# Performance work log

Measured on AMD Instinct MI355X. Metric: run time of the kernel, lower is better.

Reference implementation:

```python
import jax, jax.numpy as jnp
import numpy as np

D = 1024
H = 16
DH = D // H
F = 4096
B, S = 4, 2048
EPS = 1e-5


def _ln(x, g, b):
    m = jnp.mean(x, axis=-1, keepdims=True)
    v = jnp.var(x, axis=-1, keepdims=True)
    return (x - m) * jax.lax.rsqrt(v + EPS) * g + b


def setup_inputs() -> dict:
    key = jax.random.key(0)
    ks = jax.random.split(key, 16)
    s = 0.02
    return {
        "x": jax.random.normal(ks[0], (B, S, D), jnp.float32),
        "key_padding_mask": jnp.zeros((B, S), jnp.bool_),
        "Wq": jax.random.normal(ks[1], (D, D), jnp.float32) * s,
        "bq": jnp.zeros((D,), jnp.float32),
        "Wk": jax.random.normal(ks[2], (D, D), jnp.float32) * s,
        "bk": jnp.zeros((D,), jnp.float32),
        "Wv": jax.random.normal(ks[3], (D, D), jnp.float32) * s,
        "bv": jnp.zeros((D,), jnp.float32),
        "Wo": jax.random.normal(ks[4], (D, D), jnp.float32) * s,
        "bo": jnp.zeros((D,), jnp.float32),
        "W1": jax.random.normal(ks[5], (F, D), jnp.float32) * s,
        "b1": jnp.zeros((F,), jnp.float32),
        "W2": jax.random.normal(ks[6], (D, F), jnp.float32) * s,
        "b2": jnp.zeros((D,), jnp.float32),
        "ln1_g": jnp.ones((D,), jnp.float32),
        "ln1_b": jnp.zeros((D,), jnp.float32),
        "ln2_g": jnp.ones((D,), jnp.float32),
        "ln2_b": jnp.zeros((D,), jnp.float32),
    }


def _attn(x, kpm, Wq, bq, Wk, bk, Wv, bv, Wo, bo):
    b, s, d = x.shape
    scaling = DH ** (-0.5)
    q = (x @ Wq.T + bq) * scaling
    k = x @ Wk.T + bk
    v = x @ Wv.T + bv
    q = q.reshape(b, s, H, DH)
    k = k.reshape(b, s, H, DH)
    v = v.reshape(b, s, H, DH)
    # [b,h,q,k]
    scores = jnp.einsum("bqhd,bkhd->bhqk", q, k)
    scores = jnp.where(kpm[:, None, None, :], -jnp.inf, scores)
    p = jax.nn.softmax(scores.astype(jnp.float32), axis=-1).astype(q.dtype)
    out = jnp.einsum("bhqk,bkhd->bqhd", p, v).reshape(b, s, d)
    return out @ Wo.T + bo


def reference(x, key_padding_mask, Wq, bq, Wk, bk, Wv, bv, Wo, bo,
              W1, b1, W2, b2, ln1_g, ln1_b, ln2_g, ln2_b):
    # post-LN (normalize_before=False), dropout in eval mode (identity)
    x = _ln(x + _attn(x, key_padding_mask, Wq, bq, Wk, bk, Wv, bv, Wo, bo), ln1_g, ln1_b)
    h = jax.nn.gelu(x @ W1.T + b1, approximate=False)
    x = _ln(x + (h @ W2.T + b2), ln2_g, ln2_b)
    return x
```

## Files before the change

kernel.cpp:

```cpp
#include <hip/hip_runtime.h>
#include <hip/hip_bf16.h>
#include <math.h>

typedef short bf16x8 __attribute__((ext_vector_type(8)));
typedef float f32x4 __attribute__((ext_vector_type(4)));

__device__ __forceinline__ unsigned short f2bfu(float f) {
    __hip_bfloat16 h = __float2bfloat16(f);
    return __builtin_bit_cast(unsigned short, h);
}

__device__ __forceinline__ float fexp2(float x) {
    float r;
    asm("v_exp_f32 %0, %1" : "=v"(r) : "v"(x));
    return r;
}

__device__ __forceinline__ unsigned cvtpk_bf16(float lo, float hi) {
    unsigned r;
    asm("v_cvt_pk_bf16_f32 %0, %1, %2" : "=v"(r) : "v"(lo), "v"(hi));
    return r;
}

__device__ __forceinline__ float gelu_fast(float x) {
    const float x2 = x * x;
    const float z = x * (0.7978845608f + 0.0356774081f * x2);
    const float e = fexp2(z * 2.88539008f);
    const float r = __builtin_amdgcn_rcpf(e + 1.0f);
    return x * (1.0f - r);
}

__device__ __forceinline__ void gload_lds16(const void* gsrc, void* ldst) {
    __builtin_amdgcn_global_load_lds((const __attribute__((address_space(1))) void*)gsrc,
                                     (__attribute__((address_space(3))) void*)ldst,
                                     16, 0, 0);
}

__global__ __launch_bounds__(256)
void cvt_bf16_kernel(const float4* __restrict__ in, ushort4* __restrict__ out, int n4) {
    int i = blockIdx.x * 256 + threadIdx.x;
    if (i >= n4) return;
    float4 v = in[i];
    ushort4 o;
    o.x = f2bfu(v.x); o.y = f2bfu(v.y); o.z = f2bfu(v.z); o.w = f2bfu(v.w);
    out[i] = o;
}

enum { EPI_QKV = 0, EPI_RESF32 = 2, EPI_GELU = 3, EPI_RESBF16 = 5 };

template<int EPI>
__global__ __launch_bounds__(256, 2)
void gemm_bt(const __hip_bfloat16* __restrict__ A,
             const __hip_bfloat16* __restrict__ W,
             const float* __restrict__ bias,
             const void* __restrict__ resv,
             float scale,
             void* __restrict__ outp, void* __restrict__ outp2, void* __restrict__ outp3,
             int M, int N, int K)
{
    __shared__ __hip_bfloat16 As[2][128 * 32];
    __shared__ __hip_bfloat16 Ws[2][128 * 32];
    const int tid = threadIdx.x;
    const int lane = tid & 63;
    const int wid = tid >> 6;
    const int wr = wid >> 1, wc = wid & 1;
    const int g = lane >> 4, lr = lane & 15;
    const int row0 = blockIdx.x * 128;
    const int col0 = blockIdx.y * 128;

    f32x4 acc[4][4];
    const f32x4 zero = {0.f, 0.f, 0.f, 0.f};
#pragma unroll
    for (int m = 0; m < 4; ++m)
#pragma unroll
        for (int n = 0; n < 4; ++n) acc[m][n] = zero;

    const int c0 = tid, c1 = tid + 256;
    const int ar0 = c0 >> 2, ar1 = c1 >> 2;
    const int ac0 = ((c0 & 3) ^ ((ar0 >> 1) & 3)) * 8;
    const int ac1 = ((c1 & 3) ^ ((ar1 >> 1) & 3)) * 8;
    const __hip_bfloat16* Arow0 = A + (size_t)(row0 + ar0) * K + ac0;
    const __hip_bfloat16* Arow1 = A + (size_t)(row0 + ar1) * K + ac1;
    const __hip_bfloat16* Wrow0 = W + (size_t)(col0 + ar0) * K + ac0;
    const __hip_bfloat16* Wrow1 = W + (size_t)(col0 + ar1) * K + ac1;

    auto stage = [&](int bi, int k0) {
        gload_lds16(Arow0 + k0, (char*)As[bi] + c0 * 16);
        gload_lds16(Arow1 + k0, (char*)As[bi] + c1 * 16);
        gload_lds16(Wrow0 + k0, (char*)Ws[bi] + c0 * 16);
        gload_lds16(Wrow1 + k0, (char*)Ws[bi] + c1 * 16);
    };

    stage(0, 0);
    __syncthreads();
    int buf = 0;
    const int NT = K >> 5;
    const int swl = (lr >> 1) & 3;

    for (int t = 0; t < NT; ++t) {
        if (t + 1 < NT) stage(buf ^ 1, (t + 1) * 32);
        bf16x8 af[4], wf[4];
#pragma unroll
        for (int m = 0; m < 4; ++m)
            af[m] = *(const bf16x8*)(As[buf] + (wr * 64 + m * 16 + lr) * 32 + (g ^ swl) * 8);
#pragma unroll
        for (int n = 0; n < 4; ++n)
            wf[n] = *(const bf16x8*)(Ws[buf] + (wc * 64 + n * 16 + lr) * 32 + (g ^ swl) * 8);
#pragma unroll
        for (int m = 0; m < 4; ++m)
#pragma unroll
            for (int n = 0; n < 4; ++n)
                acc[m][n] = __builtin_amdgcn_mfma_f32_16x16x32_bf16(af[m], wf[n], acc[m][n], 0, 0, 0);
        __syncthreads();
        buf ^= 1;
    }

#pragma unroll
    for (int n = 0; n < 4; ++n) {
        const int cc = col0 + wc * 64 + n * 16 + lr;
        const float bv = bias[cc];
#pragma unroll
        for (int m = 0; m < 4; ++m) {
            const int rbase = row0 + wr * 64 + m * 16 + g * 4;
            if (EPI == EPI_QKV) {
                const int seg = col0 >> 10;
                if (seg == 2) {
                    ushort4 u;
                    u.x = f2bfu(acc[m][n][0] + bv);
                    u.y = f2bfu(acc[m][n][1] + bv);
                    u.z = f2bfu(acc[m][n][2] + bv);
                    u.w = f2bfu(acc[m][n][3] + bv);
                    const int cc2 = cc - 2048;
                    const int h_ = cc2 >> 6, dh = cc2 & 63;
                    const int bb = rbase >> 11;
                    const int s = rbase & 2047;
                    *(ushort4*)((__hip_bfloat16*)outp3 +
                                (((size_t)bb * 16 + h_) * 64 + dh) * 2048 + s) = u;
                } else {
                    const float sc = (seg == 0) ? scale : 1.0f;
                    __hip_bfloat16* dst = (seg == 0) ? (__hip_bfloat16*)outp
                                                     : (__hip_bfloat16*)outp2;
                    const int ccl = cc & 1023;
#pragma unroll
                    for (int r = 0; r < 4; ++r)
                        dst[(size_t)(rbase + r) * 1024 + ccl] =
                            __float2bfloat16((acc[m][n][r] + bv) * sc);
                }
            } else {
#pragma unroll
                for (int r = 0; r < 4; ++r) {
                    const size_t idx = (size_t)(rbase + r) * N + cc;
                    float v = acc[m][n][r] + bv;
                    if (EPI == EPI_RESF32) {
                        ((float*)outp)[idx] = v + ((const float*)resv)[idx];
                    } else if (EPI == EPI_RESBF16) {
                        ((float*)outp)[idx] = v +
                            __bfloat162float(((const __hip_bfloat16*)resv)[idx]);
                    } else if (EPI == EPI_GELU) {
                        ((__hip_bfloat16*)outp)[idx] = __float2bfloat16(gelu_fast(v));
                    }
                }
            }
        }
    }
}

__global__ __launch_bounds__(256, 2)
void attn_flash2(const __hip_bfloat16* __restrict__ Q,
                 const __hip_bfloat16* __restrict__ K,
                 const __hip_bfloat16* __restrict__ VT,
                 const unsigned char* __restrict__ kpm,
                 __hip_bfloat16* __restrict__ O)
{
    __shared__ __hip_bfloat16 Ks[2][64 * 64];
    __shared__ __hip_bfloat16 VTs[2][64 * 64];
    __shared__ __hip_bfloat16 Plds[4][64 * 64];

    const int tid = threadIdx.x;
    const int lane = tid & 63;
    const int w = tid >> 6;
    const int g = lane >> 4, lr = lane & 15;

    const int orig = blockIdx.y * 8 + blockIdx.x;
    const int nl = (orig & 7) * 64 + (orig >> 3);
    const int qb = nl & 7;
    const int bh = nl >> 3;

    const int b = bh >> 4, h = bh & 15;
    const int q0 = qb * 256 + w * 64;
    const size_t tokbase = (size_t)b * 2048;
    const __hip_bfloat16* VTbh = VT + (size_t)bh * 64 * 2048;

    bf16x8 qf[4][2];
#pragma unroll
    for (int qn = 0; qn < 4; ++qn)
#pragma unroll
        for (int f = 0; f < 2; ++f)
            qf[qn][f] = *(const bf16x8*)(Q + (tokbase + q0 + qn * 16 + lr) * 1024 +
                                         h * 64 + f * 32 + g * 8);

    f32x4 o[4][4];
    const f32x4 zero = {0.f, 0.f, 0.f, 0.f};
#pragma unroll
    for (int qa = 0; qa < 4; ++qa)
#pragma unroll
        for (int nd = 0; nd < 4; ++nd) o[qa][nd] = zero;
    float m_run[4], l_part[4];
#pragma unroll
    for (int qn = 0; qn < 4; ++qn) { m_run[qn] = -1e30f; l_part[qn] = 0.f; }

    __hip_bfloat16* Pw = Plds[w];
    const int rowl = lane >> 3;
    const int blkp = lane & 7;

    auto stage = [&](int bufi, int kv0) {
#pragma unroll
        for (int iss = 0; iss < 2; ++iss) {
            const int row = w * 16 + iss * 8 + rowl;
            const int sblk = blkp ^ (row & 7);
            gload_lds16(K + (tokbase + kv0 + row) * 1024 + h * 64 + sblk * 8,
                        (char*)&Ks[bufi][(w * 16 + iss * 8) * 64] + (lane & 63) * 16);
            gload_lds16(VTbh + (size_t)row * 2048 + kv0 + sblk * 8,
                        (char*)&VTs[bufi][(w * 16 + iss * 8) * 64] + (lane & 63) * 16);
        }
    };

    stage(0, 0);
    __syncthreads();
    int buf = 0;

    for (int t = 0; t < 32; ++t) {
        const int kv0 = t * 64;
        if (t < 31) stage(buf ^ 1, kv0 + 64);

        f32x4 st[4][4];
        __builtin_amdgcn_s_setprio(1);
#pragma unroll
        for (int km = 0; km < 4; ++km) {
            bf16x8 kf[2];
#pragma unroll
            for (int f = 0; f < 2; ++f)
                kf[f] = *(const bf16x8*)(&Ks[buf][(km * 16 + lr) * 64 +
                                                  (((f * 4 + g) ^ (lr & 7)) * 8)]);
#pragma unroll
            for (int qn = 0; qn < 4; ++qn) {
                st[km][qn] = __builtin_amdgcn_mfma_f32_16x16x32_bf16(kf[0], qf[qn][0], zero, 0, 0, 0);
                st[km][qn] = __builtin_amdgcn_mfma_f32_16x16x32_bf16(kf[1], qf[qn][1], st[km][qn], 0, 0, 0);
            }
        }
        __builtin_amdgcn_s_setprio(0);

        if (__any((int)(kpm[tokbase + kv0 + lane] != 0))) {
            const float NEG = -1e30f;
#pragma unroll
            for (int km = 0; km < 4; ++km) {
                const unsigned mu = *(const unsigned*)(kpm + tokbase + kv0 + km * 16 + g * 4);
#pragma unroll
                for (int r = 0; r < 4; ++r) {
                    if ((mu >> (8 * r)) & 0xFFu) {
#pragma unroll
                        for (int qn = 0; qn < 4; ++qn) st[km][qn][r] = NEG;
                    }
                }
            }
        }

        float pm[4];
#pragma unroll
        for (int qn = 0; qn < 4; ++qn) {
            float a0 = fmaxf(fmaxf(st[0][qn][0], st[0][qn][1]), fmaxf(st[0][qn][2], st[0][qn][3]));
            float a1 = fmaxf(fmaxf(st[1][qn][0], st[1][qn][1]), fmaxf(st[1][qn][2], st[1][qn][3]));
            float a2 = fmaxf(fmaxf(st[2][qn][0], st[2][qn][1]), fmaxf(st[2][qn][2], st[2][qn][3]));
            float a3 = fmaxf(fmaxf(st[3][qn][0], st[3][qn][1]), fmaxf(st[3][qn][2], st[3][qn][3]));
            pm[qn] = fmaxf(fmaxf(a0, a1), fmaxf(a2, a3));
        }
        const int trig = (pm[0] > m_run[0] + 8.f) | (pm[1] > m_run[1] + 8.f) |
                         (pm[2] > m_run[2] + 8.f) | (pm[3] > m_run[3] + 8.f);
        if (__any(trig)) {
            float alpha_q[4];
#pragma unroll
            for (int qn = 0; qn < 4; ++qn) {
                float rm = pm[qn];
                rm = fmaxf(rm, __shfl_xor(rm, 16));
                rm = fmaxf(rm, __shfl_xor(rm, 32));
                const float mnew = fmaxf(m_run[qn], rm);
                const float al = fexp2(m_run[qn] - mnew);
                l_part[qn] *= al;
                m_run[qn] = mnew;
                alpha_q[qn] = al;
            }
#pragma unroll
            for (int qa = 0; qa < 4; ++qa)
#pragma unroll
                for (int r = 0; r < 4; ++r) {
                    const float av = __shfl(alpha_q[qa], g * 4 + r, 16);
#pragma unroll
                    for (int nd = 0; nd < 4; ++nd) o[qa][nd][r] *= av;
                }
        }

#pragma unroll
        for (int qn = 0; qn < 4; ++qn) {
            const float mm = m_run[qn];
#pragma unroll
            for (int km = 0; km < 4; ++km) {
                const float p0 = fexp2(st[km][qn][0] - mm);
                const float p1 = fexp2(st[km][qn][1] - mm);
                const float p2 = fexp2(st[km][qn][2] - mm);
                const float p3 = fexp2(st[km][qn][3] - mm);
                l_part[qn] += (p0 + p1) + (p2 + p3);
                uint2 pk;
                pk.x = cvtpk_bf16(p0, p1);
                pk.y = cvtpk_bf16(p2, p3);
                const int cs = (km * 2 + (g >> 1)) ^ (lr & 7);
                *(uint2*)(Pw + (qn * 16 + lr) * 64 + cs * 8 + (g & 1) * 4) = pk;
            }
        }

        __builtin_amdgcn_s_setprio(1);
#pragma unroll
        for (int f = 0; f < 2; ++f) {
            bf16x8 pa[4];
#pragma unroll
            for (int qa = 0; qa < 4; ++qa)
                pa[qa] = *(const bf16x8*)(Pw + (qa * 16 + lr) * 64 +
                                          (((f * 4 + g) ^ (lr & 7)) * 8));
#pragma unroll
            for (int nd = 0; nd < 4; ++nd) {
                bf16x8 vb = *(const bf16x8*)(&VTs[buf][(nd * 16 + lr) * 64 +
                                                       (((f * 4 + g) ^ (lr & 7)) * 8)]);
#pragma unroll
                for (int qa = 0; qa < 4; ++qa)
                    o[qa][nd] = __builtin_amdgcn_mfma_f32_16x16x32_bf16(pa[qa], vb, o[qa][nd], 0, 0, 0);
            }
        }
        __builtin_amdgcn_s_setprio(0);

        __syncthreads();
        buf ^= 1;
    }

    float linv[4];
#pragma unroll
    for (int qn = 0; qn < 4; ++qn) {
        float lt = l_part[qn];
        lt += __shfl_xor(lt, 16);
        lt += __shfl_xor(lt, 32);
        linv[qn] = 1.0f / lt;
    }
#pragma unroll
    for (int qa = 0; qa < 4; ++qa)
#pragma unroll
        for (int r = 0; r < 4; ++r) {
            const float lv = __shfl(linv[qa], g * 4 + r, 16);
            const size_t row = tokbase + q0 + qa * 16 + g * 4 + r;
#pragma unroll
            for (int nd = 0; nd < 4; ++nd)
                O[row * 1024 + h * 64 + nd * 16 + lr] = __float2bfloat16(o[qa][nd][r] * lv);
        }
}

__global__ __launch_bounds__(256)
void ln_kernel(const float* __restrict__ in, const float* __restrict__ gamma,
               const float* __restrict__ beta, float* __restrict__ outf,
               __hip_bfloat16* __restrict__ outb)
{
    const int row = blockIdx.x;
    const int tid = threadIdx.x;
    float4 v = ((const float4*)(in + (size_t)row * 1024))[tid];
    float s = v.x + v.y + v.z + v.w;
    float s2 = v.x * v.x + v.y * v.y + v.z * v.z + v.w * v.w;
#pragma unroll
    for (int off = 1; off < 64; off <<= 1) {
        s += __shfl_xor(s, off);
        s2 += __shfl_xor(s2, off);
    }
    __shared__ float red[8];
    const int wv = tid >> 6;
    if ((tid & 63) == 0) { red[wv] = s; red[4 + wv] = s2; }
    __syncthreads();
    s = red[0] + red[1] + red[2] + red[3];
    s2 = red[4] + red[5] + red[6] + red[7];
    const float mean = s * (1.f / 1024.f);
    const float var = s2 * (1.f / 1024.f) - mean * mean;
    const float rstd = rsqrtf(var + 1e-5f);
    float4 gm = ((const float4*)gamma)[tid];
    float4 bt = ((const float4*)beta)[tid];
    float4 y;
    y.x = (v.x - mean) * rstd * gm.x + bt.x;
    y.y = (v.y - mean) * rstd * gm.y + bt.y;
    y.z = (v.z - mean) * rstd * gm.z + bt.z;
    y.w = (v.w - mean) * rstd * gm.w + bt.w;
    if (outf) ((float4*)(outf + (size_t)row * 1024))[tid] = y;
    if (outb) {
        ushort4 ub;
        ub.x = f2bfu(y.x); ub.y = f2bfu(y.y); ub.z = f2bfu(y.z); ub.w = f2bfu(y.w);
        ((ushort4*)outb)[row * 256 + tid] = ub;
    }
}

extern "C" void kernel_launch(void* const* d_in, const int* in_sizes, int n_in,
                              void* d_out, int out_size, void* d_ws, size_t ws_size,
                              hipStream_t stream)
{
    const float* x    = (const float*)d_in[0];
    const unsigned char* kpm = (const unsigned char*)d_in[1];
    const float* Wq = (const float*)d_in[2];
    const float* bq = (const float*)d_in[3];
    const float* Wk = (const float*)d_in[4];
    const float* bk = (const float*)d_in[5];
    const float* Wv = (const float*)d_in[6];
    const float* bv = (const float*)d_in[7];
    const float* Wo = (const float*)d_in[8];
    const float* bo = (const float*)d_in[9];
    const float* W1 = (const float*)d_in[10];
    const float* b1 = (const float*)d_in[11];
    const float* W2 = (const float*)d_in[12];
    const float* b2 = (const float*)d_in[13];
    const float* ln1g = (const float*)d_in[14];
    const float* ln1b = (const float*)d_in[15];
    const float* ln2g = (const float*)d_in[16];
    const float* ln2b = (const float*)d_in[17];
    float* out = (float*)d_out;

    char* ws = (char*)d_ws;
    const size_t SZ_ND2 = (size_t)8192 * 1024 * 2;
    size_t off = 0;
    __hip_bfloat16* xb  = (__hip_bfloat16*)(ws + off); off += SZ_ND2;
    __hip_bfloat16* wqb = (__hip_bfloat16*)(ws + off); off += (size_t)1024 * 1024 * 2;
    __hip_bfloat16* wkb = (__hip_bfloat16*)(ws + off); off += (size_t)1024 * 1024 * 2;
    __hip_bfloat16* wvb = (__hip_bfloat16*)(ws + off); off += (size_t)1024 * 1024 * 2;
    __hip_bfloat16* wob = (__hip_bfloat16*)(ws + off); off += (size_t)1024 * 1024 * 2;
    __hip_bfloat16* w1b = (__hip_bfloat16*)(ws + off); off += (size_t)4096 * 1024 * 2;
    __hip_bfloat16* w2b = (__hip_bfloat16*)(ws + off); off += (size_t)4096 * 1024 * 2;
    const size_t qkv0 = off;
    __hip_bfloat16* qbp = (__hip_bfloat16*)(ws + off); off += SZ_ND2;
    __hip_bfloat16* kbp = (__hip_bfloat16*)(ws + off); off += SZ_ND2;
    __hip_bfloat16* vtg = (__hip_bfloat16*)(ws + off); off += SZ_ND2;
    __hip_bfloat16* abp = (__hip_bfloat16*)(ws + off); off += SZ_ND2;
    __hip_bfloat16* hbp = (__hip_bfloat16*)(ws + qkv0);
    float* y1 = (float*)(ws + off); off += (size_t)8192 * 1024 * 4;
    __hip_bfloat16* x1b = (__hip_bfloat16*)(ws + off); off += SZ_ND2;
    float* y2 = y1;

    float* bqkv = (float*)(ws + off); off += 3072 * 4;

    auto cvt = [&](const float* src, void* dst, int n) {
        cvt_bf16_kernel<<<n / 1024, 256, 0, stream>>>((const float4*)src, (ushort4*)dst, n / 4);
    };
    cvt(x,  xb,  8192 * 1024);
    cvt(Wq, wqb, 1024 * 1024);
    cvt(Wk, wkb, 1024 * 1024);
    cvt(Wv, wvb, 1024 * 1024);
    cvt(Wo, wob, 1024 * 1024);
    cvt(W1, w1b, 4096 * 1024);
    cvt(W2, w2b, 4096 * 1024);
    hipMemcpyAsync(bqkv,        bq, 4096, hipMemcpyDeviceToDevice, stream);
    hipMemcpyAsync(bqkv + 1024, bk, 4096, hipMemcpyDeviceToDevice, stream);
    hipMemcpyAsync(bqkv + 2048, bv, 4096, hipMemcpyDeviceToDevice, stream);

    dim3 blk(256);

    const float qscale = 0.125f * 1.44269504088896f;
    gemm_bt<EPI_QKV><<<dim3(64, 24), blk, 0, stream>>>(
        xb, wqb, bqkv, nullptr, qscale, qbp, kbp, vtg, 8192, 3072, 1024);

    attn_flash2<<<dim3(8, 64), blk, 0, stream>>>(qbp, kbp, vtg, kpm, abp);

    gemm_bt<EPI_RESF32><<<dim3(64, 8), blk, 0, stream>>>(
        abp, wob, bo, x, 1.0f, y1, nullptr, nullptr, 8192, 1024, 1024);
    ln_kernel<<<8192, 256, 0, stream>>>(y1, ln1g, ln1b, nullptr, x1b);

    gemm_bt<EPI_GELU><<<dim3(64, 32), blk, 0, stream>>>(
        x1b, w1b, b1, nullptr, 1.0f, hbp, nullptr, nullptr, 8192, 4096, 1024);
    gemm_bt<EPI_RESBF16><<<dim3(64, 8), blk, 0, stream>>>(
        hbp, w2b, b2, x1b, 1.0f, y2, nullptr, nullptr, 8192, 1024, 4096);
    ln_kernel<<<8192, 256, 0, stream>>>(y2, ln2g, ln2b, out, nullptr);
}
```

Before: 446.1 us.

## Add 256x256 tiled GEMM kernel with interleaved LDS staging for QKV and FFN

Introduces a 512-thread GEMM kernel computing 256x256 output tiles with a K-step of 64. It overlaps direct global-to-LDS loads of the next A/B tiles with MFMA quadrants, using explicit barriers, waitcnt and priority hints. The QKV, FFN1 and FFN2 GEMMs switch to this kernel to raise arithmetic intensity and hide load latency. In exchange it needs much more LDS per block and launches far fewer blocks, which may underfill the GPU for the narrow FFN2 output.

After: 485.5 us. 1.09x slower.

```diff
diff --git a/kernel.cpp b/kernel.cpp
--- a/kernel.cpp
+++ b/kernel.cpp
@@ -35,6 +35,8 @@
                                      (__attribute__((address_space(3))) void*)ldst,
                                      16, 0, 0);
 }
+
+#define MFMA __builtin_amdgcn_mfma_f32_16x16x32_bf16
 
 __global__ __launch_bounds__(256)
 void cvt_bf16_kernel(const float4* __restrict__ in, ushort4* __restrict__ out, int n4) {
@@ -47,6 +49,199 @@
 }
 
 enum { EPI_QKV = 0, EPI_RESF32 = 2, EPI_GELU = 3, EPI_RESBF16 = 5 };
+
+template<int EPI>
+__global__ __launch_bounds__(512, 2)
+void gemm256(const __hip_bfloat16* __restrict__ A,
+             const __hip_bfloat16* __restrict__ W,
+             const float* __restrict__ bias,
+             const void* __restrict__ resv,
+             float scale,
+             void* __restrict__ outp, void* __restrict__ outp2, void* __restrict__ outp3,
+             int M, int N, int K)
+{
+    __shared__ __hip_bfloat16 Asb[2][256 * 64];
+    __shared__ __hip_bfloat16 Bsb[2][256 * 64];
+    const int tid = threadIdx.x;
+    const int l = tid & 63;
+    const int wid = tid >> 6;
+    const int wr = wid >> 2;
+    const int wc = wid & 3;
+    const int g = l >> 4, lr = l & 15;
+    const int row0 = blockIdx.x * 256;
+    const int col0 = blockIdx.y * 256;
+
+    const int hb = wc >> 1;
+    const int qb = wr * 2 + (wc & 1);
+    const int arowq = wr * 128 + wc * 32;
+    const int browq = hb * 128 + qb * 32;
+    const int sblk = ((l & 7) ^ (l >> 3)) * 8;
+    const __hip_bfloat16* Asrc = A + (size_t)(row0 + arowq + (l >> 3)) * K + sblk;
+    const __hip_bfloat16* Wsrc = W + (size_t)(col0 + browq + (l >> 3)) * K + sblk;
+    const int aldst = arowq * 128 + l * 16;
+    const int bldst = browq * 128 + l * 16;
+
+    auto stageA = [&](int bi, int kt) {
+#pragma unroll
+        for (int i = 0; i < 4; ++i)
+            gload_lds16(Asrc + (size_t)(i * 8) * K + kt * 64,
+                        (char*)Asb[bi] + aldst + i * 1024);
+    };
+    auto stageB = [&](int bi, int kt) {
+#pragma unroll
+        for (int i = 0; i < 4; ++i)
+            gload_lds16(Wsrc + (size_t)(i * 8) * K + kt * 64,
+                        (char*)Bsb[bi] + bldst + i * 1024);
+    };
+
+    f32x4 acc[8][4];
+    const f32x4 zero = {0.f, 0.f, 0.f, 0.f};
+#pragma unroll
+    for (int m = 0; m < 8; ++m)
+#pragma unroll
+        for (int n = 0; n < 4; ++n) acc[m][n] = zero;
+
+    const int sw = lr & 7;
+    const int NT = K >> 6;
+
+    stageA(0, 0); stageB(0, 0); stageA(1, 1);
+    asm volatile("s_waitcnt vmcnt(4)" ::: "memory");
+    __builtin_amdgcn_s_barrier();
+    __builtin_amdgcn_sched_barrier(0);
+
+    for (int kt = 0; kt < NT; ++kt) {
+        const int b = kt & 1;
+        const __hip_bfloat16* Ab = Asb[b];
+        const __hip_bfloat16* Bb = Bsb[b];
+        bf16x8 a4[4][2], b01[2][2], b23[2][2];
+
+#pragma unroll
+        for (int m = 0; m < 4; ++m)
+#pragma unroll
+            for (int ks = 0; ks < 2; ++ks)
+                a4[m][ks] = *(const bf16x8*)((const char*)Ab +
+                    (wr * 128 + m * 16 + lr) * 128 + (((ks * 4 + g) ^ sw) * 16));
+#pragma unroll
+        for (int n = 0; n < 2; ++n)
+#pragma unroll
+            for (int ks = 0; ks < 2; ++ks)
+                b01[n][ks] = *(const bf16x8*)((const char*)Bb +
+                    (wc * 64 + n * 16 + lr) * 128 + (((ks * 4 + g) ^ sw) * 16));
+        if (kt + 1 < NT) stageB(b ^ 1, kt + 1);
+        __builtin_amdgcn_s_barrier();
+        __builtin_amdgcn_s_setprio(1);
+#pragma unroll
+        for (int m = 0; m < 4; ++m)
+#pragma unroll
+            for (int n = 0; n < 2; ++n) {
+                acc[m][n] = MFMA(a4[m][0], b01[n][0], acc[m][n], 0, 0, 0);
+                acc[m][n] = MFMA(a4[m][1], b01[n][1], acc[m][n], 0, 0, 0);
+            }
+        __builtin_amdgcn_s_setprio(0);
+        __builtin_amdgcn_s_barrier();
+
+#pragma unroll
+        for (int n = 0; n < 2; ++n)
+#pragma unroll
+            for (int ks = 0; ks < 2; ++ks)
+                b23[n][ks] = *(const bf16x8*)((const char*)Bb +
+                    (wc * 64 + (n + 2) * 16 + lr) * 128 + (((ks * 4 + g) ^ sw) * 16));
+        __builtin_amdgcn_s_barrier();
+        __builtin_amdgcn_s_setprio(1);
+#pragma unroll
+        for (int m = 0; m < 4; ++m)
+#pragma unroll
+            for (int n = 0; n < 2; ++n) {
+                acc[m][n + 2] = MFMA(a4[m][0], b23[n][0], acc[m][n + 2], 0, 0, 0);
+                acc[m][n + 2] = MFMA(a4[m][1], b23[n][1], acc[m][n + 2], 0, 0, 0);
+            }
+        __builtin_amdgcn_s_setprio(0);
+        __builtin_amdgcn_s_barrier();
+
+#pragma unroll
+        for (int m = 0; m < 4; ++m)
+#pragma unroll
+            for (int ks = 0; ks < 2; ++ks)
+                a4[m][ks] = *(const bf16x8*)((const char*)Ab +
+                    (wr * 128 + (m + 4) * 16 + lr) * 128 + (((ks * 4 + g) ^ sw) * 16));
+        __builtin_amdgcn_s_barrier();
+        __builtin_amdgcn_s_setprio(1);
+#pragma unroll
+        for (int m = 0; m < 4; ++m)
+#pragma unroll
+            for (int n = 0; n < 2; ++n) {
+                acc[m + 4][n + 2] = MFMA(a4[m][0], b23[n][0], acc[m + 4][n + 2], 0, 0, 0);
+                acc[m + 4][n + 2] = MFMA(a4[m][1], b23[n][1], acc[m + 4][n + 2], 0, 0, 0);
+            }
+        __builtin_amdgcn_s_setprio(0);
+        __builtin_amdgcn_s_barrier();
+
+        if (kt + 2 < NT) stageA(b, kt + 2);
+        __builtin_amdgcn_s_barrier();
+        __builtin_amdgcn_s_setprio(1);
+#pragma unroll
+        for (int m = 0; m < 4; ++m)
+#pragma unroll
+            for (int n = 0; n < 2; ++n) {
+                acc[m + 4][n] = MFMA(a4[m][0], b01[n][0], acc[m + 4][n], 0, 0, 0);
+                acc[m + 4][n] = MFMA(a4[m][1], b01[n][1], acc[m + 4][n], 0, 0, 0);
+            }
+        __builtin_amdgcn_s_setprio(0);
+        if (kt + 2 < NT) asm volatile("s_waitcnt vmcnt(4)" ::: "memory");
+        else             asm volatile("s_waitcnt vmcnt(0)" ::: "memory");
+        __builtin_amdgcn_s_barrier();
+        __builtin_amdgcn_sched_barrier(0);
+    }
+
+#pragma unroll
+    for (int n = 0; n < 4; ++n) {
+        const int cc = col0 + wc * 64 + n * 16 + lr;
+        const float bv = bias[cc];
+#pragma unroll
+        for (int m = 0; m < 8; ++m) {
+            const int rbase = row0 + wr * 128 + m * 16 + g * 4;
+            if (EPI == EPI_QKV) {
+                const int seg = col0 >> 10;
+                if (seg == 2) {
+                    ushort4 u;
+                    u.x = f2bfu(acc[m][n][0] + bv);
+                    u.y = f2bfu(acc[m][n][1] + bv);
+                    u.z = f2bfu(acc[m][n][2] + bv);
+                    u.w = f2bfu(acc[m][n][3] + bv);
+                    const int cc2 = cc - 2048;
+                    const int h_ = cc2 >> 6, dh = cc2 & 63;
+                    const int bb = rbase >> 11;
+                    const int s = rbase & 2047;
+                    *(ushort4*)((__hip_bfloat16*)outp3 +
+                                (((size_t)bb * 16 + h_) * 64 + dh) * 2048 + s) = u;
+                } else {
+                    const float sc = (seg == 0) ? scale : 1.0f;
+                    __hip_bfloat16* dst = (seg == 0) ? (__hip_bfloat16*)outp
+                                                     : (__hip_bfloat16*)outp2;
+                    const int ccl = cc & 1023;
+#pragma unroll
+                    for (int r = 0; r < 4; ++r)
+                        dst[(size_t)(rbase + r) * 1024 + ccl] =
+                            __float2bfloat16((acc[m][n][r] + bv) * sc);
+                }
+            } else {
+#pragma unroll
+                for (int r = 0; r < 4; ++r) {
+                    const size_t idx = (size_t)(rbase + r) * N + cc;
+                    float v = acc[m][n][r] + bv;
+                    if (EPI == EPI_RESF32) {
+                        ((float*)outp)[idx] = v + ((const float*)resv)[idx];
+                    } else if (EPI == EPI_RESBF16) {
+                        ((float*)outp)[idx] = v +
+                            __bfloat162float(((const __hip_bfloat16*)resv)[idx]);
+                    } else if (EPI == EPI_GELU) {
+                        ((__hip_bfloat16*)outp)[idx] = __float2bfloat16(gelu_fast(v));
+                    }
+                }
+            }
+        }
+    }
+}
 
 template<int EPI>
 __global__ __launch_bounds__(256, 2)
@@ -110,7 +305,7 @@
         for (int m = 0; m < 4; ++m)
 #pragma unroll
             for (int n = 0; n < 4; ++n)
-                acc[m][n] = __builtin_amdgcn_mfma_f32_16x16x32_bf16(af[m], wf[n], acc[m][n], 0, 0, 0);
+                acc[m][n] = MFMA(af[m], wf[n], acc[m][n], 0, 0, 0);
         __syncthreads();
         buf ^= 1;
     }
@@ -122,43 +317,17 @@
 #pragma unroll
         for (int m = 0; m < 4; ++m) {
             const int rbase = row0 + wr * 64 + m * 16 + g * 4;
-            if (EPI == EPI_QKV) {
-                const int seg = col0 >> 10;
-                if (seg == 2) {
-                    ushort4 u;
-                    u.x = f2bfu(acc[m][n][0] + bv);
-                    u.y = f2bfu(acc[m][n][1] + bv);
-                    u.z = f2bfu(acc[m][n][2] + bv);
-                    u.w = f2bfu(acc[m][n][3] + bv);
-                    const int cc2 = cc - 2048;
-                    const int h_ = cc2 >> 6, dh = cc2 & 63;
-                    const int bb = rbase >> 11;
-                    const int s = rbase & 2047;
-                    *(ushort4*)((__hip_bfloat16*)outp3 +
-                                (((size_t)bb * 16 + h_) * 64 + dh) * 2048 + s) = u;
-                } else {
-                    const float sc = (seg == 0) ? scale : 1.0f;
-                    __hip_bfloat16* dst = (seg == 0) ? (__hip_bfloat16*)outp
-                                                     : (__hip_bfloat16*)outp2;
-                    const int ccl = cc & 1023;
-#pragma unroll
-                    for (int r = 0; r < 4; ++r)
-                        dst[(size_t)(rbase + r) * 1024 + ccl] =
-                            __float2bfloat16((acc[m][n][r] + bv) * sc);
-                }
-            } else {
-#pragma unroll
-                for (int r = 0; r < 4; ++r) {
-                    const size_t idx = (size_t)(rbase + r) * N + cc;
-                    float v = acc[m][n][r] + bv;
-                    if (EPI == EPI_RESF32) {
-                        ((float*)outp)[idx] = v + ((const float*)resv)[idx];
-                    } else if (EPI == EPI_RESBF16) {
-                        ((float*)outp)[idx] = v +
-                            __bfloat162float(((const __hip_bfloat16*)resv)[idx]);
-                    } else if (EPI == EPI_GELU) {
-                        ((__hip_bfloat16*)outp)[idx] = __float2bfloat16(gelu_fast(v));
-                    }
+#pragma unroll
+            for (int r = 0; r < 4; ++r) {
+                const size_t idx = (size_t)(rbase + r) * N + cc;
+                float v = acc[m][n][r] + bv;
+                if (EPI == EPI_RESF32) {
+                    ((float*)outp)[idx] = v + ((const float*)resv)[idx];
+                } else if (EPI == EPI_RESBF16) {
+                    ((float*)outp)[idx] = v +
+                        __bfloat162float(((const __hip_bfloat16*)resv)[idx]);
+                } else if (EPI == EPI_GELU) {
+                    ((__hip_bfloat16*)outp)[idx] = __float2bfloat16(gelu_fast(v));
                 }
             }
         }
@@ -244,8 +413,8 @@
                                                   (((f * 4 + g) ^ (lr & 7)) * 8)]);
 #pragma unroll
             for (int qn = 0; qn < 4; ++qn) {
-                st[km][qn] = __builtin_amdgcn_mfma_f32_16x16x32_bf16(kf[0], qf[qn][0], zero, 0, 0, 0);
-                st[km][qn] = __builtin_amdgcn_mfma_f32_16x16x32_bf16(kf[1], qf[qn][1], st[km][qn], 0, 0, 0);
+                st[km][qn] = MFMA(kf[0], qf[qn][0], zero, 0, 0, 0);
+                st[km][qn] = MFMA(kf[1], qf[qn][1], st[km][qn], 0, 0, 0);
             }
         }
         __builtin_amdgcn_s_setprio(0);
@@ -331,7 +500,7 @@
                                                        (((f * 4 + g) ^ (lr & 7)) * 8)]);
 #pragma unroll
                 for (int qa = 0; qa < 4; ++qa)
-                    o[qa][nd] = __builtin_amdgcn_mfma_f32_16x16x32_bf16(pa[qa], vb, o[qa][nd], 0, 0, 0);
+                    o[qa][nd] = MFMA(pa[qa], vb, o[qa][nd], 0, 0, 0);
             }
         }
         __builtin_amdgcn_s_setprio(0);
@@ -442,7 +611,6 @@
     float* y1 = (float*)(ws + off); off += (size_t)8192 * 1024 * 4;
     __hip_bfloat16* x1b = (__hip_bfloat16*)(ws + off); off += SZ_ND2;
     float* y2 = y1;
-
     float* bqkv = (float*)(ws + off); off += 3072 * 4;
 
     auto cvt = [&](const float* src, void* dst, int n) {
@@ -459,21 +627,20 @@
     hipMemcpyAsync(bqkv + 1024, bk, 4096, hipMemcpyDeviceToDevice, stream);
     hipMemcpyAsync(bqkv + 2048, bv, 4096, hipMemcpyDeviceToDevice, stream);
 
-    dim3 blk(256);
-
     const float qscale = 0.125f * 1.44269504088896f;
-    gemm_bt<EPI_QKV><<<dim3(64, 24), blk, 0, stream>>>(
+
+    gemm256<EPI_QKV><<<dim3(32, 12), 512, 0, stream>>>(
         xb, wqb, bqkv, nullptr, qscale, qbp, kbp, vtg, 8192, 3072, 1024);
 
-    attn_flash2<<<dim3(8, 64), blk, 0, stream>>>(qbp, kbp, vtg, kpm, abp);
-
-    gemm_bt<EPI_RESF32><<<dim3(64, 8), blk, 0, stream>>>(
+    attn_flash2<<<dim3(8, 64), 256, 0, stream>>>(qbp, kbp, vtg, kpm, abp);
+
+    gemm_bt<EPI_RESF32><<<dim3(64, 8), 256, 0, stream>>>(
         abp, wob, bo, x, 1.0f, y1, nullptr, nullptr, 8192, 1024, 1024);
     ln_kernel<<<8192, 256, 0, stream>>>(y1, ln1g, ln1b, nullptr, x1b);
 
-    gemm_bt<EPI_GELU><<<dim3(64, 32), blk, 0, stream>>>(
+    gemm256<EPI_GELU><<<dim3(32, 16), 512, 0, stream>>>(
         x1b, w1b, b1, nullptr, 1.0f, hbp, nullptr, nullptr, 8192, 4096, 1024);
-    gemm_bt<EPI_RESBF16><<<dim3(64, 8), blk, 0, stream>>>(
+    gemm256<EPI_RESBF16><<<dim3(32, 4), 512, 0, stream>>>(
         hbp, w2b, b2, x1b, 1.0f, y2, nullptr, nullptr, 8192, 1024, 4096);
     ln_kernel<<<8192, 256, 0, stream>>>(y2, ln2g, ln2b, out, nullptr);
 }
```
